# Optimization experiments

Measured on AMD Instinct MI355X. Metric: run time of the kernel, lower is better.

## Reference

```python
import jax, jax.numpy as jnp
import numpy as np

HID = 256
IN_DIM = 256
OUT_DIM = 10
L_CYCLES = 6
H_CYCLES = 3
BATCH = 131072
LN_EPS = 1e-5


def _layernorm(v, w, b):
    mu = jnp.mean(v, axis=-1, keepdims=True)
    var = jnp.mean(jnp.square(v - mu), axis=-1, keepdims=True)
    return (v - mu) * jax.lax.rsqrt(var + LN_EPS) * w + b


def setup_inputs() -> dict:
    key = jax.random.key(0)
    ks = jax.random.split(key, 12)
    s = lambda fan_in: 1.0 / np.sqrt(fan_in)
    inp = {
        "x": jax.random.normal(ks[0], (BATCH, IN_DIM), dtype=jnp.float32),
        "W_in": jax.random.uniform(ks[1], (IN_DIM, HID), jnp.float32, -s(IN_DIM), s(IN_DIM)),
        "b_in": jnp.zeros((HID,), jnp.float32),
        "y_init": jax.random.normal(ks[2], (1, HID), dtype=jnp.float32) * 0.02,
        "W_up": jax.random.uniform(ks[3], (HID, 4 * HID), jnp.float32, -s(HID), s(HID)),
        "b_up": jnp.zeros((4 * HID,), jnp.float32),
        "W_down": jax.random.uniform(ks[4], (4 * HID, HID), jnp.float32, -s(4 * HID), s(4 * HID)),
        "b_down": jnp.zeros((HID,), jnp.float32),
        "ln_w": jnp.ones((HID,), jnp.float32),
        "ln_b": jnp.zeros((HID,), jnp.float32),
        "W_comb": jax.random.uniform(ks[5], (2 * HID, HID), jnp.float32, -s(2 * HID), s(2 * HID)),
        "b_comb": jnp.zeros((HID,), jnp.float32),
        "W_yt": jax.random.uniform(ks[6], (HID, HID), jnp.float32, -s(HID), s(HID)),
        "b_yt": jnp.zeros((HID,), jnp.float32),
        "W_head": jax.random.uniform(ks[7], (HID, OUT_DIM), jnp.float32, -s(HID), s(HID)),
        "b_head": jnp.zeros((OUT_DIM,), jnp.float32),
    }
    return inp


def reference(x, W_in, b_in, y_init, W_up, b_up, W_down, b_down, ln_w, ln_b,
              W_comb, b_comb, W_yt, b_yt, W_head, b_head):
    z = x @ W_in + b_in                      # [B, H]
    y = jnp.broadcast_to(y_init, (x.shape[0], HID))
    for _ in range(H_CYCLES):
        for _ in range(L_CYCLES):
            h = jax.nn.gelu(z @ W_up + b_up, approximate=False)
            h = h @ W_down + b_down
            z = _layernorm(z + h, ln_w, ln_b)
        combined = jnp.concatenate([z, y], axis=-1)   # [B, 2H]
        h = jax.nn.gelu(combined @ W_comb + b_comb, approximate=False)
        y = y + h @ W_yt + b_yt
    return y @ W_head + b_head
```

## Files before the change

kernel.cpp:

```cpp
#include <hip/hip_runtime.h>

typedef _Float16 h16;
typedef h16 h16x8 __attribute__((ext_vector_type(8)));
typedef float f32x4 __attribute__((ext_vector_type(4)));

#define MFMA16(a, b, c) __builtin_amdgcn_mfma_f32_16x16x32_f16(a, b, c, 0, 0, 0)

typedef __attribute__((address_space(1))) const char gconst_char;
typedef __attribute__((address_space(3))) char lds_char;
#define GL_LDS16(g, l) __builtin_amdgcn_global_load_lds((gconst_char*)(g), (lds_char*)(l), 16, 0, 0)

#define WIN_OFF   0
#define WIN_CSH   17408
#define WUP_OFF   (WIN_OFF + 8 * WIN_CSH)
#define WUP_CSH   17408
#define WDN_OFF   (WUP_OFF + 32 * WUP_CSH)
#define WDN_CSH   16384
#define WCOMB_OFF (WDN_OFF + 32 * WDN_CSH)
#define WCOMB_CSH 33792
#define WYT_OFF   (WCOMB_OFF + 8 * WCOMB_CSH)
#define WYT_CSH   16384
#define WHEAD_OFF (WYT_OFF + 8 * WYT_CSH)
#define WHEAD_SZ  9216
#define ZY_OFF    (WHEAD_OFF + WHEAD_SZ)
#define ZY_BYTES  (131072UL * 512UL * 2UL)

#define L_WUP0 0
#define L_WUP1 17408
#define L_WDN0 34816
#define L_WDN1 51200
#define L_HS   67584
#define SMEM_MEGA 77824

#define C_WC0 0
#define C_WC1 33792
#define C_WY0 67584
#define C_WY1 83968
#define C_GS  100352
#define SMEM_COMB 120832

#define SMEM_HEAD 9216

__device__ __forceinline__ void stage_calls(const char* src, char* dst, int calls, int wave,
                                            int nw, int lane) {
  for (int i = wave; i < calls; i += nw)
    GL_LDS16(src + i * 1024 + lane * 16, dst + i * 1024);
}

__device__ __forceinline__ float gelu_f(float x) {
  float t = x * (2.3021177f + 0.1029434f * x * x);
  float e = __builtin_amdgcn_exp2f(-t);
  return x * __builtin_amdgcn_rcpf(1.0f + e);
}

__global__ void prepA_kernel(const float* __restrict__ src, h16* __restrict__ dst,
                             int K, int KPp, int CHN, int Nsrc, int CSHh, int tot) {
  for (int d = blockIdx.x * 256 + threadIdx.x; d < tot; d += gridDim.x * 256) {
    int chunk = d / CSHh, r = d % CSHh;
    float v = 0.0f;
    if (r < CHN * KPp) {
      int nl = r / KPp, k = r % KPp;
      int n = chunk * CHN + nl;
      if (k < K && n < Nsrc) v = src[(long)k * Nsrc + n];
    }
    dst[d] = (h16)v;
  }
}
__global__ void prepB_kernel(const float* __restrict__ src, h16* __restrict__ dst,
                             int Kc, int KP2p, int N, int CSHh, int tot) {
  for (int d = blockIdx.x * 256 + threadIdx.x; d < tot; d += gridDim.x * 256) {
    int chunk = d / CSHh, r = d % CSHh;
    float v = 0.0f;
    if (r < N * KP2p) {
      int n = r / KP2p, kp = r % KP2p;
      if (kp < Kc) v = src[(long)(chunk * Kc + kp) * N + n];
    }
    dst[d] = (h16)v;
  }
}

__global__ __launch_bounds__(256, 2) void mega_kernel(
    const float* x, h16* zy,
    const char* __restrict__ winP, const char* __restrict__ wupP, const char* __restrict__ wdnP,
    const float* __restrict__ b_in, const float* __restrict__ b_up,
    const float* __restrict__ b_down, const float* __restrict__ ln_w,
    const float* __restrict__ ln_b, int first) {
  extern __shared__ char smem[];
  const int tid = threadIdx.x, wave = tid >> 6, lane = tid & 63;
  const int q = lane >> 4, c = lane & 15;
  const long m0 = (long)blockIdx.x * 128 + wave * 32;

  f32x4 acc2[2][16];
  h16x8 az[2][8];
  h16* hsH = (h16*)(smem + L_HS + wave * 2560);
  h16* zth = (h16*)(smem) + wave * 4224;
  const f32x4 vzero = {0.0f, 0.0f, 0.0f, 0.0f};

  if (first) {
#pragma unroll
    for (int rt = 0; rt < 2; ++rt)
#pragma unroll
      for (int kk = 0; kk < 8; ++kk) {
        const float* p = x + (m0 + rt * 16 + c) * 256 + kk * 32 + q * 8;
        f32x4 u0 = *(const f32x4*)p;
        f32x4 u1 = *(const f32x4*)(p + 4);
        h16x8 a;
        a[0] = (h16)u0[0]; a[1] = (h16)u0[1]; a[2] = (h16)u0[2]; a[3] = (h16)u0[3];
        a[4] = (h16)u1[0]; a[5] = (h16)u1[1]; a[6] = (h16)u1[2]; a[7] = (h16)u1[3];
        az[rt][kk] = a;
      }
#pragma unroll
    for (int rt = 0; rt < 2; ++rt)
#pragma unroll
      for (int nt = 0; nt < 16; ++nt) acc2[rt][nt] = vzero;

    stage_calls(winP, smem + L_WUP0, 17, wave, 4, lane);
    __syncthreads();
#pragma unroll
    for (int ncI = 0; ncI < 8; ++ncI) {
      if (ncI < 7)
        stage_calls(winP + (ncI + 1) * WIN_CSH, smem + (((ncI + 1) & 1) ? L_WUP1 : L_WUP0),
                    17, wave, 4, lane);
      const char* wb = smem + ((ncI & 1) ? L_WUP1 : L_WUP0);
#pragma unroll
      for (int kk = 0; kk < 8; ++kk)
#pragma unroll
        for (int nt = 0; nt < 2; ++nt) {
          h16x8 b = *(const h16x8*)(wb + ((nt * 16 + c) * 264 + kk * 32 + q * 8) * 2);
#pragma unroll
          for (int rt = 0; rt < 2; ++rt)
            acc2[rt][ncI * 2 + nt] = MFMA16(az[rt][kk], b, acc2[rt][ncI * 2 + nt]);
        }
      __syncthreads();
    }
#pragma unroll
    for (int nt = 0; nt < 16; ++nt) {
      float bi = b_in[nt * 16 + c];
#pragma unroll
      for (int rt = 0; rt < 2; ++rt)
#pragma unroll
        for (int r = 0; r < 4; ++r) acc2[rt][nt][r] += bi;
    }
  } else {
#pragma unroll
    for (int rt = 0; rt < 2; ++rt) {
#pragma unroll
      for (int kk = 0; kk < 8; ++kk) {
        az[rt][kk] = *(const h16x8*)(zy + (m0 + rt * 16 + c) * 512 + kk * 32 + q * 8);
        *(h16x8*)(zth + c * 264 + kk * 32 + q * 8) = az[rt][kk];
      }
#pragma unroll
      for (int nt = 0; nt < 16; ++nt)
#pragma unroll
        for (int r = 0; r < 4; ++r)
          acc2[rt][nt][r] = (float)zth[(q * 4 + r) * 264 + nt * 16 + c];
    }
  }

  for (int it = 0; it < 6; ++it) {
    if (it > 0 || first) {
#pragma unroll
      for (int rt = 0; rt < 2; ++rt) {
#pragma unroll
        for (int nt = 0; nt < 16; ++nt)
#pragma unroll
          for (int r = 0; r < 4; ++r)
            zth[(q * 4 + r) * 264 + nt * 16 + c] = (h16)acc2[rt][nt][r];
#pragma unroll
        for (int kk = 0; kk < 8; ++kk)
          az[rt][kk] = *(const h16x8*)(zth + c * 264 + kk * 32 + q * 8);
      }
    }
    __syncthreads();
    stage_calls(wupP, smem + L_WUP0, 17, wave, 4, lane);
    stage_calls(wdnP, smem + L_WDN0, 16, wave, 4, lane);
    __syncthreads();

    for (int nc = 0; nc < 32; ++nc) {
      if (nc < 31) {
        int nb = (nc + 1) & 1;
        stage_calls(wupP + (nc + 1) * WUP_CSH, smem + (nb ? L_WUP1 : L_WUP0), 17, wave, 4, lane);
        stage_calls(wdnP + (nc + 1) * WDN_CSH, smem + (nb ? L_WDN1 : L_WDN0), 16, wave, 4, lane);
      }
      const char* wub = smem + ((nc & 1) ? L_WUP1 : L_WUP0);
      const char* wdb = smem + ((nc & 1) ? L_WDN1 : L_WDN0);

      f32x4 acc1[2][2];
      acc1[0][0] = vzero; acc1[0][1] = vzero; acc1[1][0] = vzero; acc1[1][1] = vzero;
#pragma unroll
      for (int kk = 0; kk < 8; ++kk)
#pragma unroll
        for (int nt = 0; nt < 2; ++nt) {
          h16x8 b = *(const h16x8*)(wub + ((nt * 16 + c) * 264 + kk * 32 + q * 8) * 2);
#pragma unroll
          for (int rt = 0; rt < 2; ++rt) acc1[rt][nt] = MFMA16(az[rt][kk], b, acc1[rt][nt]);
        }
      float bu0 = b_up[nc * 32 + c];
      float bu1 = b_up[nc * 32 + 16 + c];
#pragma unroll
      for (int rt = 0; rt < 2; ++rt)
#pragma unroll
        for (int nt = 0; nt < 2; ++nt) {
          float bu = nt ? bu1 : bu0;
#pragma unroll
          for (int r = 0; r < 4; ++r) {
            float g = gelu_f(acc1[rt][nt][r] + bu);
            hsH[(rt * 16 + q * 4 + r) * 40 + nt * 16 + c] = (h16)g;
          }
        }
      h16x8 ah[2];
#pragma unroll
      for (int rt = 0; rt < 2; ++rt)
        ah[rt] = *(const h16x8*)(hsH + (rt * 16 + c) * 40 + q * 8);
#pragma unroll
      for (int nt = 0; nt < 16; ++nt) {
        h16x8 b = *(const h16x8*)(wdb + ((nt * 16 + c) * 32 + q * 8) * 2);
#pragma unroll
        for (int rt = 0; rt < 2; ++rt) acc2[rt][nt] = MFMA16(ah[rt], b, acc2[rt][nt]);
      }
      __syncthreads();
    }

#pragma unroll
    for (int rt = 0; rt < 2; ++rt) {
      float sum[4] = {0, 0, 0, 0}, sq[4] = {0, 0, 0, 0};
#pragma unroll
      for (int nt = 0; nt < 16; ++nt) {
        float bd = b_down[nt * 16 + c];
#pragma unroll
        for (int r = 0; r < 4; ++r) {
          float v = acc2[rt][nt][r] + bd;
          acc2[rt][nt][r] = v;
          sum[r] += v;
          sq[r] += v * v;
        }
      }
#pragma unroll
      for (int r = 0; r < 4; ++r)
#pragma unroll
        for (int m = 1; m < 16; m <<= 1) {
          sum[r] += __shfl_xor(sum[r], m, 16);
          sq[r] += __shfl_xor(sq[r], m, 16);
        }
      float mu[4], rs[4];
#pragma unroll
      for (int r = 0; r < 4; ++r) {
        mu[r] = sum[r] * (1.0f / 256.0f);
        float var = sq[r] * (1.0f / 256.0f) - mu[r] * mu[r];
        rs[r] = __builtin_amdgcn_rsqf(var + 1e-5f);
      }
#pragma unroll
      for (int nt = 0; nt < 16; ++nt) {
        float w = ln_w[nt * 16 + c], bb = ln_b[nt * 16 + c];
#pragma unroll
        for (int r = 0; r < 4; ++r)
          acc2[rt][nt][r] = (acc2[rt][nt][r] - mu[r]) * rs[r] * w + bb;
      }
    }
  }

#pragma unroll
  for (int rt = 0; rt < 2; ++rt) {
#pragma unroll
    for (int nt = 0; nt < 16; ++nt)
#pragma unroll
      for (int r = 0; r < 4; ++r)
        zth[(q * 4 + r) * 264 + nt * 16 + c] = (h16)acc2[rt][nt][r];
#pragma unroll
    for (int kk = 0; kk < 8; ++kk) {
      h16x8 v = *(const h16x8*)(zth + c * 264 + kk * 32 + q * 8);
      *(h16x8*)(zy + (m0 + rt * 16 + c) * 512 + kk * 32 + q * 8) = v;
    }
  }
}

__global__ __launch_bounds__(512) void comb_kernel(
    h16* zy, const char* __restrict__ wcP, const char* __restrict__ wytP,
    const float* __restrict__ b_comb, const float* __restrict__ b_yt,
    const float* __restrict__ y_init, int first) {
  extern __shared__ char smem[];
  const int tid = threadIdx.x, wave = tid >> 6, lane = tid & 63;
  const int q = lane >> 4, c = lane & 15;
  const long m0 = (long)blockIdx.x * 256 + wave * 32;

  h16* gsH = (h16*)(smem + C_GS + wave * 2560);
  h16* yth = (h16*)(smem) + wave * 4224;

  f32x4 acc2[2][16];
  if (first) {
#pragma unroll
    for (int nt = 0; nt < 16; ++nt) {
      float yv = y_init[nt * 16 + c];
#pragma unroll
      for (int rt = 0; rt < 2; ++rt)
#pragma unroll
        for (int r = 0; r < 4; ++r) acc2[rt][nt][r] = yv;
    }
  } else {
#pragma unroll
    for (int rt = 0; rt < 2; ++rt) {
#pragma unroll
      for (int kk = 0; kk < 8; ++kk) {
        h16x8 v = *(const h16x8*)(zy + (m0 + rt * 16 + c) * 512 + 256 + kk * 32 + q * 8);
        *(h16x8*)(yth + c * 264 + kk * 32 + q * 8) = v;
      }
#pragma unroll
      for (int nt = 0; nt < 16; ++nt)
#pragma unroll
        for (int r = 0; r < 4; ++r)
          acc2[rt][nt][r] = (float)yth[(q * 4 + r) * 264 + nt * 16 + c];
    }
  }
  __syncthreads();
  const f32x4 vzero = {0.0f, 0.0f, 0.0f, 0.0f};

  stage_calls(wcP, smem + C_WC0, 33, wave, 8, lane);
  stage_calls(wytP, smem + C_WY0, 16, wave, 8, lane);
  __syncthreads();

  for (int nc = 0; nc < 8; ++nc) {
    if (nc < 7) {
      int nb = (nc + 1) & 1;
      stage_calls(wcP + (nc + 1) * WCOMB_CSH, smem + (nb ? C_WC1 : C_WC0), 33, wave, 8, lane);
      stage_calls(wytP + (nc + 1) * WYT_CSH, smem + (nb ? C_WY1 : C_WY0), 16, wave, 8, lane);
    }
    const char* wcb = smem + ((nc & 1) ? C_WC1 : C_WC0);
    const char* wyb = smem + ((nc & 1) ? C_WY1 : C_WY0);

    f32x4 acc1[2][2];
    acc1[0][0] = vzero; acc1[0][1] = vzero; acc1[1][0] = vzero; acc1[1][1] = vzero;
#pragma unroll
    for (int kk = 0; kk < 16; ++kk) {
      h16x8 a[2];
#pragma unroll
      for (int rt = 0; rt < 2; ++rt)
        a[rt] = *(const h16x8*)(zy + (m0 + rt * 16 + c) * 512 + kk * 32 + q * 8);
#pragma unroll
      for (int nt = 0; nt < 2; ++nt) {
        h16x8 b = *(const h16x8*)(wcb + ((nt * 16 + c) * 520 + kk * 32 + q * 8) * 2);
#pragma unroll
        for (int rt = 0; rt < 2; ++rt) acc1[rt][nt] = MFMA16(a[rt], b, acc1[rt][nt]);
      }
    }
    float bc0 = b_comb[nc * 32 + c];
    float bc1 = b_comb[nc * 32 + 16 + c];
#pragma unroll
    for (int rt = 0; rt < 2; ++rt)
#pragma unroll
      for (int nt = 0; nt < 2; ++nt) {
        float bc = nt ? bc1 : bc0;
#pragma unroll
        for (int r = 0; r < 4; ++r) {
          float g = gelu_f(acc1[rt][nt][r] + bc);
          gsH[(rt * 16 + q * 4 + r) * 40 + nt * 16 + c] = (h16)g;
        }
      }
    h16x8 ah[2];
#pragma unroll
    for (int rt = 0; rt < 2; ++rt)
      ah[rt] = *(const h16x8*)(gsH + (rt * 16 + c) * 40 + q * 8);
#pragma unroll
    for (int nt = 0; nt < 16; ++nt) {
      h16x8 b = *(const h16x8*)(wyb + ((nt * 16 + c) * 32 + q * 8) * 2);
#pragma unroll
      for (int rt = 0; rt < 2; ++rt) acc2[rt][nt] = MFMA16(ah[rt], b, acc2[rt][nt]);
    }
    __syncthreads();
  }

#pragma unroll
  for (int rt = 0; rt < 2; ++rt) {
#pragma unroll
    for (int nt = 0; nt < 16; ++nt) {
      float by = b_yt[nt * 16 + c];
#pragma unroll
      for (int r = 0; r < 4; ++r)
        yth[(q * 4 + r) * 264 + nt * 16 + c] = (h16)(acc2[rt][nt][r] + by);
    }
#pragma unroll
    for (int kk = 0; kk < 8; ++kk) {
      h16x8 v = *(const h16x8*)(yth + c * 264 + kk * 32 + q * 8);
      *(h16x8*)(zy + (m0 + rt * 16 + c) * 512 + 256 + kk * 32 + q * 8) = v;
    }
  }
}

__global__ __launch_bounds__(256) void head_kernel(const h16* zy, const char* __restrict__ whP,
                                                   const float* __restrict__ b_head,
                                                   float* __restrict__ out) {
  extern __shared__ char smem[];
  const int tid = threadIdx.x, wave = tid >> 6, lane = tid & 63;
  const int q = lane >> 4, c = lane & 15;
  const long m0 = (long)blockIdx.x * 128 + wave * 32;

  stage_calls(whP, smem, 9, wave, 4, lane);
  __syncthreads();

  f32x4 acc[2];
  const f32x4 vzero = {0.0f, 0.0f, 0.0f, 0.0f};
  acc[0] = vzero; acc[1] = vzero;
#pragma unroll
  for (int kk = 0; kk < 8; ++kk) {
    h16x8 b = *(const h16x8*)(smem + (c * 264 + kk * 32 + q * 8) * 2);
#pragma unroll
    for (int rt = 0; rt < 2; ++rt) {
      h16x8 a = *(const h16x8*)(zy + (m0 + rt * 16 + c) * 512 + 256 + kk * 32 + q * 8);
      acc[rt] = MFMA16(a, b, acc[rt]);
    }
  }
  if (c < 10) {
    float bh = b_head[c];
#pragma unroll
    for (int rt = 0; rt < 2; ++rt)
#pragma unroll
      for (int r = 0; r < 4; ++r)
        out[(m0 + rt * 16 + q * 4 + r) * 10 + c] = acc[rt][r] + bh;
  }
}

extern "C" void kernel_launch(void* const* d_in, const int* in_sizes, int n_in, void* d_out,
                              int out_size, void* d_ws, size_t ws_size, hipStream_t stream) {
  (void)in_sizes; (void)n_in; (void)out_size;
  const float* x      = (const float*)d_in[0];
  const float* W_in   = (const float*)d_in[1];
  const float* b_in   = (const float*)d_in[2];
  const float* y_init = (const float*)d_in[3];
  const float* W_up   = (const float*)d_in[4];
  const float* b_up   = (const float*)d_in[5];
  const float* W_down = (const float*)d_in[6];
  const float* b_down = (const float*)d_in[7];
  const float* ln_w   = (const float*)d_in[8];
  const float* ln_b   = (const float*)d_in[9];
  const float* W_comb = (const float*)d_in[10];
  const float* b_comb = (const float*)d_in[11];
  const float* W_yt   = (const float*)d_in[12];
  const float* b_yt   = (const float*)d_in[13];
  const float* W_head = (const float*)d_in[14];
  const float* b_head = (const float*)d_in[15];

  char* ws = (char*)d_ws;
  h16* winP   = (h16*)(ws + WIN_OFF);
  h16* wupP   = (h16*)(ws + WUP_OFF);
  h16* wdnP   = (h16*)(ws + WDN_OFF);
  h16* wcombP = (h16*)(ws + WCOMB_OFF);
  h16* wytP   = (h16*)(ws + WYT_OFF);
  h16* wheadP = (h16*)(ws + WHEAD_OFF);
  h16* zy = (ws_size >= (size_t)ZY_OFF + ZY_BYTES) ? (h16*)(ws + ZY_OFF) : (h16*)d_in[0];

  hipFuncSetAttribute((const void*)mega_kernel, hipFuncAttributeMaxDynamicSharedMemorySize,
                      SMEM_MEGA);
  hipFuncSetAttribute((const void*)comb_kernel, hipFuncAttributeMaxDynamicSharedMemorySize,
                      SMEM_COMB);

  {
    int tot;
    tot = 8 * (WIN_CSH / 2);
    prepA_kernel<<<dim3((tot + 255) / 256), dim3(256), 0, stream>>>(W_in, winP, 256, 264, 32, 256, WIN_CSH / 2, tot);
    tot = 32 * (WUP_CSH / 2);
    prepA_kernel<<<dim3((tot + 255) / 256), dim3(256), 0, stream>>>(W_up, wupP, 256, 264, 32, 1024, WUP_CSH / 2, tot);
    tot = 8 * (WCOMB_CSH / 2);
    prepA_kernel<<<dim3((tot + 255) / 256), dim3(256), 0, stream>>>(W_comb, wcombP, 512, 520, 32, 256, WCOMB_CSH / 2, tot);
    tot = WHEAD_SZ / 2;
    prepA_kernel<<<dim3((tot + 255) / 256), dim3(256), 0, stream>>>(W_head, wheadP, 256, 264, 16, 10, WHEAD_SZ / 2, tot);
    tot = 32 * (WDN_CSH / 2);
    prepB_kernel<<<dim3((tot + 255) / 256), dim3(256), 0, stream>>>(W_down, wdnP, 32, 32, 256, WDN_CSH / 2, tot);
    tot = 8 * (WYT_CSH / 2);
    prepB_kernel<<<dim3((tot + 255) / 256), dim3(256), 0, stream>>>(W_yt, wytP, 32, 32, 256, WYT_CSH / 2, tot);
  }

  for (int h = 0; h < 3; ++h) {
    mega_kernel<<<dim3(1024), dim3(256), SMEM_MEGA, stream>>>(
        x, zy, (const char*)winP, (const char*)wupP, (const char*)wdnP, b_in, b_up, b_down,
        ln_w, ln_b, (h == 0) ? 1 : 0);
    comb_kernel<<<dim3(512), dim3(512), SMEM_COMB, stream>>>(
        zy, (const char*)wcombP, (const char*)wytP, b_comb, b_yt, y_init, (h == 0) ? 1 : 0);
  }
  head_kernel<<<dim3(1024), dim3(256), SMEM_HEAD, stream>>>(zy, (const char*)wheadP, b_head,
                                                            (float*)d_out);
}
```

Measured before the change: 4.169 ms.

## Single-buffer W_up staging, swizzle GELU tile, pad W_down, cache biases in LDS

The FFN loop now stages W_up into a single LDS buffer, refilled after the up-projection MFMAs and a barrier. W_down stays double-buffered with its row stride padded from 32 to 40 halves, and the GELU scratch tile uses an XOR swizzle to reduce LDS bank conflicts. Biases and layernorm parameters are cached in LDS, and the kernel is split into first and resume variants sharing an inlined body. The intent is less LDS per block and fewer bank conflicts, at the cost of an extra barrier per chunk and less overlap between the W_up load and compute.

```diff
diff --git a/kernel.cpp b/kernel.cpp
--- a/kernel.cpp
+++ b/kernel.cpp
@@ -10,27 +10,30 @@
 typedef __attribute__((address_space(3))) char lds_char;
 #define GL_LDS16(g, l) __builtin_amdgcn_global_load_lds((gconst_char*)(g), (lds_char*)(l), 16, 0, 0)
 
+#define WIN_CSH   16896
 #define WIN_OFF   0
-#define WIN_CSH   17408
-#define WUP_OFF   (WIN_OFF + 8 * WIN_CSH)
-#define WUP_CSH   17408
-#define WDN_OFF   (WUP_OFF + 32 * WUP_CSH)
-#define WDN_CSH   16384
-#define WCOMB_OFF (WDN_OFF + 32 * WDN_CSH)
+#define WUP_CSH   16896
+#define WUP_OFF   135168
+#define WDN_CSH   20480
+#define WDN_OFF   675840
 #define WCOMB_CSH 33792
-#define WYT_OFF   (WCOMB_OFF + 8 * WCOMB_CSH)
+#define WCOMB_OFF 1331200
 #define WYT_CSH   16384
-#define WHEAD_OFF (WYT_OFF + 8 * WYT_CSH)
+#define WYT_OFF   1601536
+#define WHEAD_OFF 1732608
 #define WHEAD_SZ  9216
-#define ZY_OFF    (WHEAD_OFF + WHEAD_SZ)
+#define ZY_OFF    1741824
 #define ZY_BYTES  (131072UL * 512UL * 2UL)
 
-#define L_WUP0 0
-#define L_WUP1 17408
-#define L_WDN0 34816
-#define L_WDN1 51200
-#define L_HS   67584
-#define SMEM_MEGA 77824
+#define L_WUP  0
+#define L_WDN0 16896
+#define L_WDN1 37376
+#define L_HS   57856
+#define L_BUP  68096
+#define L_BDN  72192
+#define L_LNW  73216
+#define L_LNB  74240
+#define SMEM_MEGA 75264
 
 #define C_WC0 0
 #define C_WC1 33792
@@ -45,6 +48,12 @@
                                             int nw, int lane) {
   for (int i = wave; i < calls; i += nw)
     GL_LDS16(src + i * 1024 + lane * 16, dst + i * 1024);
+}
+__device__ __forceinline__ void stage_wup(const char* src, char* dst, int wave, int lane) {
+  for (int i = wave; i < 17; i += 4) {
+    if (i < 16) GL_LDS16(src + i * 1024 + lane * 16, dst + i * 1024);
+    else if (lane < 32) GL_LDS16(src + 16384 + lane * 16, dst + 16384);
+  }
 }
 
 __device__ __forceinline__ float gelu_f(float x) {
@@ -79,86 +88,27 @@
   }
 }
 
-__global__ __launch_bounds__(256, 2) void mega_kernel(
-    const float* x, h16* zy,
-    const char* __restrict__ winP, const char* __restrict__ wupP, const char* __restrict__ wdnP,
-    const float* __restrict__ b_in, const float* __restrict__ b_up,
-    const float* __restrict__ b_down, const float* __restrict__ ln_w,
-    const float* __restrict__ ln_b, int first) {
-  extern __shared__ char smem[];
-  const int tid = threadIdx.x, wave = tid >> 6, lane = tid & 63;
-  const int q = lane >> 4, c = lane & 15;
-  const long m0 = (long)blockIdx.x * 128 + wave * 32;
-
-  f32x4 acc2[2][16];
-  h16x8 az[2][8];
+__device__ __forceinline__ void ffn_body(
+    char* smem, h16* zy, const char* wupP, const char* wdnP,
+    const float* b_up, const float* b_down, const float* ln_w, const float* ln_b,
+    f32x4 (&acc2)[2][16], h16x8 (&az)[2][8],
+    int tid, int wave, int lane, int q, int c, long m0, int zt0) {
   h16* hsH = (h16*)(smem + L_HS + wave * 2560);
-  h16* zth = (h16*)(smem) + wave * 4224;
+  h16* zth = (h16*)smem + wave * 4224;
+  float* bupL = (float*)(smem + L_BUP);
+  float* bdnL = (float*)(smem + L_BDN);
+  float* lnwL = (float*)(smem + L_LNW);
+  float* lnbL = (float*)(smem + L_LNB);
+  const int cq2 = (c >> 2) & 3;
   const f32x4 vzero = {0.0f, 0.0f, 0.0f, 0.0f};
 
-  if (first) {
-#pragma unroll
-    for (int rt = 0; rt < 2; ++rt)
-#pragma unroll
-      for (int kk = 0; kk < 8; ++kk) {
-        const float* p = x + (m0 + rt * 16 + c) * 256 + kk * 32 + q * 8;
-        f32x4 u0 = *(const f32x4*)p;
-        f32x4 u1 = *(const f32x4*)(p + 4);
-        h16x8 a;
-        a[0] = (h16)u0[0]; a[1] = (h16)u0[1]; a[2] = (h16)u0[2]; a[3] = (h16)u0[3];
-        a[4] = (h16)u1[0]; a[5] = (h16)u1[1]; a[6] = (h16)u1[2]; a[7] = (h16)u1[3];
-        az[rt][kk] = a;
-      }
-#pragma unroll
-    for (int rt = 0; rt < 2; ++rt)
-#pragma unroll
-      for (int nt = 0; nt < 16; ++nt) acc2[rt][nt] = vzero;
-
-    stage_calls(winP, smem + L_WUP0, 17, wave, 4, lane);
-    __syncthreads();
-#pragma unroll
-    for (int ncI = 0; ncI < 8; ++ncI) {
-      if (ncI < 7)
-        stage_calls(winP + (ncI + 1) * WIN_CSH, smem + (((ncI + 1) & 1) ? L_WUP1 : L_WUP0),
-                    17, wave, 4, lane);
-      const char* wb = smem + ((ncI & 1) ? L_WUP1 : L_WUP0);
-#pragma unroll
-      for (int kk = 0; kk < 8; ++kk)
-#pragma unroll
-        for (int nt = 0; nt < 2; ++nt) {
-          h16x8 b = *(const h16x8*)(wb + ((nt * 16 + c) * 264 + kk * 32 + q * 8) * 2);
-#pragma unroll
-          for (int rt = 0; rt < 2; ++rt)
-            acc2[rt][ncI * 2 + nt] = MFMA16(az[rt][kk], b, acc2[rt][ncI * 2 + nt]);
-        }
-      __syncthreads();
-    }
-#pragma unroll
-    for (int nt = 0; nt < 16; ++nt) {
-      float bi = b_in[nt * 16 + c];
-#pragma unroll
-      for (int rt = 0; rt < 2; ++rt)
-#pragma unroll
-        for (int r = 0; r < 4; ++r) acc2[rt][nt][r] += bi;
-    }
-  } else {
-#pragma unroll
-    for (int rt = 0; rt < 2; ++rt) {
-#pragma unroll
-      for (int kk = 0; kk < 8; ++kk) {
-        az[rt][kk] = *(const h16x8*)(zy + (m0 + rt * 16 + c) * 512 + kk * 32 + q * 8);
-        *(h16x8*)(zth + c * 264 + kk * 32 + q * 8) = az[rt][kk];
-      }
-#pragma unroll
-      for (int nt = 0; nt < 16; ++nt)
-#pragma unroll
-        for (int r = 0; r < 4; ++r)
-          acc2[rt][nt][r] = (float)zth[(q * 4 + r) * 264 + nt * 16 + c];
-    }
-  }
+  for (int i = tid; i < 1024; i += 256) bupL[i] = b_up[i];
+  bdnL[tid] = b_down[tid];
+  lnwL[tid] = ln_w[tid];
+  lnbL[tid] = ln_b[tid];
 
   for (int it = 0; it < 6; ++it) {
-    if (it > 0 || first) {
+    if (it > 0 || zt0) {
 #pragma unroll
       for (int rt = 0; rt < 2; ++rt) {
 #pragma unroll
@@ -172,51 +122,62 @@
       }
     }
     __syncthreads();
-    stage_calls(wupP, smem + L_WUP0, 17, wave, 4, lane);
-    stage_calls(wdnP, smem + L_WDN0, 16, wave, 4, lane);
+    stage_wup(wupP, smem + L_WUP, wave, lane);
+    stage_calls(wdnP, smem + L_WDN0, 20, wave, 4, lane);
     __syncthreads();
 
     for (int nc = 0; nc < 32; ++nc) {
+      const char* wub = smem + L_WUP;
+      const char* wdb = smem + ((nc & 1) ? L_WDN1 : L_WDN0);
+
+      f32x4 p00 = vzero, p01 = vzero, p10 = vzero, p11 = vzero;
+#pragma unroll
+      for (int kk = 0; kk < 8; ++kk) {
+        h16x8 b = *(const h16x8*)(wub + (c * 264 + kk * 32 + q * 8) * 2);
+        p00 = MFMA16(az[0][kk], b, p00);
+        p01 = MFMA16(az[1][kk], b, p01);
+      }
+      __builtin_amdgcn_sched_barrier(0);
+#pragma unroll
+      for (int kk = 0; kk < 8; ++kk) {
+        h16x8 b = *(const h16x8*)(wub + ((16 + c) * 264 + kk * 32 + q * 8) * 2);
+        p10 = MFMA16(az[0][kk], b, p10);
+        p11 = MFMA16(az[1][kk], b, p11);
+      }
+      __syncthreads();
       if (nc < 31) {
-        int nb = (nc + 1) & 1;
-        stage_calls(wupP + (nc + 1) * WUP_CSH, smem + (nb ? L_WUP1 : L_WUP0), 17, wave, 4, lane);
-        stage_calls(wdnP + (nc + 1) * WDN_CSH, smem + (nb ? L_WDN1 : L_WDN0), 16, wave, 4, lane);
-      }
-      const char* wub = smem + ((nc & 1) ? L_WUP1 : L_WUP0);
-      const char* wdb = smem + ((nc & 1) ? L_WDN1 : L_WDN0);
-
-      f32x4 acc1[2][2];
-      acc1[0][0] = vzero; acc1[0][1] = vzero; acc1[1][0] = vzero; acc1[1][1] = vzero;
-#pragma unroll
-      for (int kk = 0; kk < 8; ++kk)
-#pragma unroll
-        for (int nt = 0; nt < 2; ++nt) {
-          h16x8 b = *(const h16x8*)(wub + ((nt * 16 + c) * 264 + kk * 32 + q * 8) * 2);
-#pragma unroll
-          for (int rt = 0; rt < 2; ++rt) acc1[rt][nt] = MFMA16(az[rt][kk], b, acc1[rt][nt]);
-        }
-      float bu0 = b_up[nc * 32 + c];
-      float bu1 = b_up[nc * 32 + 16 + c];
-#pragma unroll
-      for (int rt = 0; rt < 2; ++rt)
-#pragma unroll
-        for (int nt = 0; nt < 2; ++nt) {
-          float bu = nt ? bu1 : bu0;
-#pragma unroll
-          for (int r = 0; r < 4; ++r) {
-            float g = gelu_f(acc1[rt][nt][r] + bu);
-            hsH[(rt * 16 + q * 4 + r) * 40 + nt * 16 + c] = (h16)g;
-          }
-        }
-      h16x8 ah[2];
-#pragma unroll
-      for (int rt = 0; rt < 2; ++rt)
-        ah[rt] = *(const h16x8*)(hsH + (rt * 16 + c) * 40 + q * 8);
-#pragma unroll
-      for (int nt = 0; nt < 16; ++nt) {
-        h16x8 b = *(const h16x8*)(wdb + ((nt * 16 + c) * 32 + q * 8) * 2);
-#pragma unroll
-        for (int rt = 0; rt < 2; ++rt) acc2[rt][nt] = MFMA16(ah[rt], b, acc2[rt][nt]);
+        stage_wup(wupP + (nc + 1) * WUP_CSH, smem + L_WUP, wave, lane);
+        stage_calls(wdnP + (nc + 1) * WDN_CSH,
+                    smem + (((nc + 1) & 1) ? L_WDN1 : L_WDN0), 20, wave, 4, lane);
+      }
+
+      float bu0 = bupL[nc * 32 + c];
+      float bu1 = bupL[nc * 32 + 16 + c];
+      const int ksw0 = c ^ (q * 8);
+      const int ksw1 = (16 + c) ^ (q * 8);
+#pragma unroll
+      for (int r = 0; r < 4; ++r) {
+        hsH[(q * 4 + r) * 40 + ksw0]      = (h16)gelu_f(p00[r] + bu0);
+        hsH[(16 + q * 4 + r) * 40 + ksw0] = (h16)gelu_f(p01[r] + bu0);
+        hsH[(q * 4 + r) * 40 + ksw1]      = (h16)gelu_f(p10[r] + bu1);
+        hsH[(16 + q * 4 + r) * 40 + ksw1] = (h16)gelu_f(p11[r] + bu1);
+      }
+      const int krd = (q ^ cq2) * 8;
+      h16x8 ah0 = *(const h16x8*)(hsH + c * 40 + krd);
+      h16x8 ah1 = *(const h16x8*)(hsH + (16 + c) * 40 + krd);
+
+#pragma unroll
+      for (int nt = 0; nt < 8; ++nt) {
+        h16x8 b = *(const h16x8*)(wdb + ((nt * 16 + c) * 40 + q * 8) * 2);
+        acc2[0][nt] = MFMA16(ah0, b, acc2[0][nt]);
+        acc2[1][nt] = MFMA16(ah1, b, acc2[1][nt]);
+      }
+      __builtin_amdgcn_sched_barrier(0);
+#pragma unroll
+      for (int nt = 8; nt < 16; ++nt) {
+        h16x8 b = *(const h16x8*)(wdb + ((nt * 16 + c) * 40 + q * 8) * 2);
+        acc2[0][nt] = MFMA16(ah0, b, acc2[0][nt]);
+        acc2[1][nt] = MFMA16(ah1, b, acc2[1][nt]);
       }
       __syncthreads();
     }
@@ -226,7 +187,7 @@
       float sum[4] = {0, 0, 0, 0}, sq[4] = {0, 0, 0, 0};
 #pragma unroll
       for (int nt = 0; nt < 16; ++nt) {
-        float bd = b_down[nt * 16 + c];
+        float bd = bdnL[nt * 16 + c];
 #pragma unroll
         for (int r = 0; r < 4; ++r) {
           float v = acc2[rt][nt][r] + bd;
@@ -251,7 +212,7 @@
       }
 #pragma unroll
       for (int nt = 0; nt < 16; ++nt) {
-        float w = ln_w[nt * 16 + c], bb = ln_b[nt * 16 + c];
+        float w = lnwL[nt * 16 + c], bb = lnbL[nt * 16 + c];
 #pragma unroll
         for (int r = 0; r < 4; ++r)
           acc2[rt][nt][r] = (acc2[rt][nt][r] - mu[r]) * rs[r] * w + bb;
@@ -272,6 +233,104 @@
       *(h16x8*)(zy + (m0 + rt * 16 + c) * 512 + kk * 32 + q * 8) = v;
     }
   }
+}
+
+__global__ __launch_bounds__(256, 2) void mega_first(
+    const float* __restrict__ x, h16* zy,
+    const char* __restrict__ winP, const char* __restrict__ wupP, const char* __restrict__ wdnP,
+    const float* __restrict__ b_in, const float* __restrict__ b_up,
+    const float* __restrict__ b_down, const float* __restrict__ ln_w,
+    const float* __restrict__ ln_b) {
+  extern __shared__ char smem[];
+  const int tid = threadIdx.x, wave = tid >> 6, lane = tid & 63;
+  const int q = lane >> 4, c = lane & 15;
+  const long m0 = (long)blockIdx.x * 128 + wave * 32;
+
+  f32x4 acc2[2][16];
+  h16x8 az[2][8];
+  const f32x4 vzero = {0.0f, 0.0f, 0.0f, 0.0f};
+
+#pragma unroll
+  for (int rt = 0; rt < 2; ++rt)
+#pragma unroll
+    for (int kk = 0; kk < 8; ++kk) {
+      const float* p = x + (m0 + rt * 16 + c) * 256 + kk * 32 + q * 8;
+      f32x4 u0 = *(const f32x4*)p;
+      f32x4 u1 = *(const f32x4*)(p + 4);
+      h16x8 a;
+      a[0] = (h16)u0[0]; a[1] = (h16)u0[1]; a[2] = (h16)u0[2]; a[3] = (h16)u0[3];
+      a[4] = (h16)u1[0]; a[5] = (h16)u1[1]; a[6] = (h16)u1[2]; a[7] = (h16)u1[3];
+      az[rt][kk] = a;
+    }
+#pragma unroll
+  for (int rt = 0; rt < 2; ++rt)
+#pragma unroll
+    for (int nt = 0; nt < 16; ++nt) acc2[rt][nt] = vzero;
+
+  stage_wup(winP, smem + L_WUP, wave, lane);
+  __syncthreads();
+#pragma unroll
+  for (int ncI = 0; ncI < 8; ++ncI) {
+#pragma unroll
+    for (int kk = 0; kk < 8; ++kk) {
+      h16x8 b = *(const h16x8*)(smem + L_WUP + (c * 264 + kk * 32 + q * 8) * 2);
+      acc2[0][ncI * 2] = MFMA16(az[0][kk], b, acc2[0][ncI * 2]);
+      acc2[1][ncI * 2] = MFMA16(az[1][kk], b, acc2[1][ncI * 2]);
+    }
+    __builtin_amdgcn_sched_barrier(0);
+#pragma unroll
+    for (int kk = 0; kk < 8; ++kk) {
+      h16x8 b = *(const h16x8*)(smem + L_WUP + ((16 + c) * 264 + kk * 32 + q * 8) * 2);
+      acc2[0][ncI * 2 + 1] = MFMA16(az[0][kk], b, acc2[0][ncI * 2 + 1]);
+      acc2[1][ncI * 2 + 1] = MFMA16(az[1][kk], b, acc2[1][ncI * 2 + 1]);
+    }
+    __syncthreads();
+    if (ncI < 7) stage_wup(winP + (ncI + 1) * WIN_CSH, smem + L_WUP, wave, lane);
+    __syncthreads();
+  }
+#pragma unroll
+  for (int nt = 0; nt < 16; ++nt) {
+    float bi = b_in[nt * 16 + c];
+#pragma unroll
+    for (int rt = 0; rt < 2; ++rt)
+#pragma unroll
+      for (int r = 0; r < 4; ++r) acc2[rt][nt][r] += bi;
+  }
+
+  ffn_body(smem, zy, wupP, wdnP, b_up, b_down, ln_w, ln_b, acc2, az,
+           tid, wave, lane, q, c, m0, 1);
+}
+
+__global__ __launch_bounds__(256, 2) void mega_resume(
+    h16* zy,
+    const char* __restrict__ wupP, const char* __restrict__ wdnP,
+    const float* __restrict__ b_up, const float* __restrict__ b_down,
+    const float* __restrict__ ln_w, const float* __restrict__ ln_b) {
+  extern __shared__ char smem[];
+  const int tid = threadIdx.x, wave = tid >> 6, lane = tid & 63;
+  const int q = lane >> 4, c = lane & 15;
+  const long m0 = (long)blockIdx.x * 128 + wave * 32;
+
+  f32x4 acc2[2][16];
+  h16x8 az[2][8];
+  h16* zth = (h16*)smem + wave * 4224;
+
+#pragma unroll
+  for (int rt = 0; rt < 2; ++rt) {
+#pragma unroll
+    for (int kk = 0; kk < 8; ++kk) {
+      az[rt][kk] = *(const h16x8*)(zy + (m0 + rt * 16 + c) * 512 + kk * 32 + q * 8);
+      *(h16x8*)(zth + c * 264 + kk * 32 + q * 8) = az[rt][kk];
+    }
+#pragma unroll
+    for (int nt = 0; nt < 16; ++nt)
+#pragma unroll
+      for (int r = 0; r < 4; ++r)
+        acc2[rt][nt][r] = (float)zth[(q * 4 + r) * 264 + nt * 16 + c];
+  }
+
+  ffn_body(smem, zy, wupP, wdnP, b_up, b_down, ln_w, ln_b, acc2, az,
+           tid, wave, lane, q, c, m0, 0);
 }
 
 __global__ __launch_bounds__(512) void comb_kernel(
@@ -447,7 +506,9 @@
   h16* wheadP = (h16*)(ws + WHEAD_OFF);
   h16* zy = (ws_size >= (size_t)ZY_OFF + ZY_BYTES) ? (h16*)(ws + ZY_OFF) : (h16*)d_in[0];
 
-  hipFuncSetAttribute((const void*)mega_kernel, hipFuncAttributeMaxDynamicSharedMemorySize,
+  hipFuncSetAttribute((const void*)mega_first, hipFuncAttributeMaxDynamicSharedMemorySize,
+                      SMEM_MEGA);
+  hipFuncSetAttribute((const void*)mega_resume, hipFuncAttributeMaxDynamicSharedMemorySize,
                       SMEM_MEGA);
   hipFuncSetAttribute((const void*)comb_kernel, hipFuncAttributeMaxDynamicSharedMemorySize,
                       SMEM_COMB);
@@ -463,15 +524,19 @@
     tot = WHEAD_SZ / 2;
     prepA_kernel<<<dim3((tot + 255) / 256), dim3(256), 0, stream>>>(W_head, wheadP, 256, 264, 16, 10, WHEAD_SZ / 2, tot);
     tot = 32 * (WDN_CSH / 2);
-    prepB_kernel<<<dim3((tot + 255) / 256), dim3(256), 0, stream>>>(W_down, wdnP, 32, 32, 256, WDN_CSH / 2, tot);
+    prepB_kernel<<<dim3((tot + 255) / 256), dim3(256), 0, stream>>>(W_down, wdnP, 32, 40, 256, WDN_CSH / 2, tot);
     tot = 8 * (WYT_CSH / 2);
     prepB_kernel<<<dim3((tot + 255) / 256), dim3(256), 0, stream>>>(W_yt, wytP, 32, 32, 256, WYT_CSH / 2, tot);
   }
 
   for (int h = 0; h < 3; ++h) {
-    mega_kernel<<<dim3(1024), dim3(256), SMEM_MEGA, stream>>>(
-        x, zy, (const char*)winP, (const char*)wupP, (const char*)wdnP, b_in, b_up, b_down,
-        ln_w, ln_b, (h == 0) ? 1 : 0);
+    if (h == 0)
+      mega_first<<<dim3(1024), dim3(256), SMEM_MEGA, stream>>>(
+          x, zy, (const char*)winP, (const char*)wupP, (const char*)wdnP,
+          b_in, b_up, b_down, ln_w, ln_b);
+    else
+      mega_resume<<<dim3(1024), dim3(256), SMEM_MEGA, stream>>>(
+          zy, (const char*)wupP, (const char*)wdnP, b_up, b_down, ln_w, ln_b);
     comb_kernel<<<dim3(512), dim3(512), SMEM_COMB, stream>>>(
         zy, (const char*)wcombP, (const char*)wytP, b_comb, b_yt, y_init, (h == 0) ? 1 : 0);
   }
```

New measurement: 5.782 ms. +38.7%, slower.
